# Kernel optimization log

Hardware: AMD Instinct MI355X
Metric: run time of the kernel (lower is better)

Reference implementation:

```python
import jax, jax.numpy as jnp
import numpy as np

NUM_ITERATIONS = 5
USE_SYMMETRIC_FINAL = True


def setup_inputs() -> dict:
    key = jax.random.key(0)
    k1, _ = jax.random.split(key)
    log_scores = jax.random.normal(k1, (4, 16, 1024, 1024), dtype=jnp.float32)
    tau = jnp.float32(1.0)
    return {"log_scores": log_scores, "tau": tau}


def reference(log_scores, tau):
    # tau clamped to min 0.1 as in torch .clamp(min=0.1)
    tau_c = jnp.maximum(tau, jnp.float32(0.1))
    ls = log_scores / tau_c
    # Sinkhorn iterations: alternate row / column logsumexp normalization.
    for _ in range(NUM_ITERATIONS):
        ls = ls - jax.nn.logsumexp(ls, axis=-1, keepdims=True)  # row normalize
        ls = ls - jax.nn.logsumexp(ls, axis=-2, keepdims=True)  # col normalize
    if USE_SYMMETRIC_FINAL:
        ls = ls - jax.nn.logsumexp(ls, axis=-1, keepdims=True)
        ls_col = ls - jax.nn.logsumexp(ls, axis=-2, keepdims=True)
        ls = 0.5 * (ls + ls_col)
    return jnp.exp(ls)
```

## Files before the change

kernel.cpp:

```cpp
#include <hip/hip_runtime.h>
#include <hip/hip_fp16.h>


#define NROWS 1024
#define NCOLS 1024
#define NMAT 64
#define MATELEMS (NROWS * NCOLS)

struct H8 { __half2 h[4]; };

__device__ __forceinline__ float wave_sum(float v) {
#pragma unroll
  for (int o = 32; o > 0; o >>= 1) v += __shfl_xor(v, o, 64);
  return v;
}

__global__ __launch_bounds__(256) void convert_row(
    const float* __restrict__ x, __half* __restrict__ t,
    float* __restrict__ r, const float* __restrict__ tau) {
  const float it = 1.0f / fmaxf(tau[0], 0.1f);
  const int row = blockIdx.x * 4 + (threadIdx.x >> 6);
  const int lane = threadIdx.x & 63;
  const float4* xr = (const float4*)(x + (size_t)row * NCOLS);
  H8* tr = (H8*)(t + (size_t)row * NCOLS);
  float s = 0.0f;
#pragma unroll
  for (int k = 0; k < 2; ++k) {
    const int f4 = k * 128 + lane * 2;
    float4 a = xr[f4];
    float4 b = xr[f4 + 1];
    a.x *= it; a.y *= it; a.z *= it; a.w *= it;
    b.x *= it; b.y *= it; b.z *= it; b.w *= it;
    H8 o;
    o.h[0] = __floats2half2_rn(a.x, a.y);
    o.h[1] = __floats2half2_rn(a.z, a.w);
    o.h[2] = __floats2half2_rn(b.x, b.y);
    o.h[3] = __floats2half2_rn(b.z, b.w);
    tr[k * 64 + lane] = o;
    s += __expf(a.x) + __expf(a.y) + __expf(a.z) + __expf(a.w) +
         __expf(b.x) + __expf(b.y) + __expf(b.z) + __expf(b.w);
  }
  s = wave_sum(s);
  if (lane == 0) r[row] = __logf(s);
}

__global__ __launch_bounds__(256) void row_pass(
    const __half* __restrict__ t, const float* __restrict__ c,
    float* __restrict__ r) {
  const int row = blockIdx.x * 4 + (threadIdx.x >> 6);
  const int lane = threadIdx.x & 63;
  const int mat = row >> 10;
  const H8* tr = (const H8*)(t + (size_t)row * NCOLS);
  const float4* cm = (const float4*)(c + mat * NCOLS);
  float s = 0.0f;
#pragma unroll
  for (int k = 0; k < 2; ++k) {
    H8 v = tr[k * 64 + lane];
    const int f4 = k * 128 + lane * 2;
    float4 c0 = cm[f4];
    float4 c1 = cm[f4 + 1];
    float2 f0 = __half22float2(v.h[0]);
    float2 f1 = __half22float2(v.h[1]);
    float2 f2 = __half22float2(v.h[2]);
    float2 f3 = __half22float2(v.h[3]);
    s += __expf(f0.x - c0.x) + __expf(f0.y - c0.y) +
         __expf(f1.x - c0.z) + __expf(f1.y - c0.w) +
         __expf(f2.x - c1.x) + __expf(f2.y - c1.y) +
         __expf(f3.x - c1.z) + __expf(f3.y - c1.w);
  }
  s = wave_sum(s);
  if (lane == 0) r[row] = __logf(s);
}

template <int FUSE>
__global__ __launch_bounds__(256) void col_pass(
    const __half* __restrict__ t, const float* __restrict__ r,
    const float* __restrict__ cin, float* __restrict__ cout,
    float* __restrict__ out) {
  const int mat = blockIdx.x >> 3;
  const int cb = blockIdx.x & 7;
  const int colh = threadIdx.x & 15;
  const int rg = threadIdx.x >> 4;
  const int h8idx = cb * 16 + colh;
  const __half* tb = t + (size_t)mat * MATELEMS;
  const float* rb = r + mat * NROWS;

  float s[8];
#pragma unroll
  for (int j = 0; j < 8; ++j) s[j] = 0.0f;

  for (int rr = 0; rr < 64; ++rr) {
    const int row = rg * 64 + rr;
    H8 v = ((const H8*)(tb + (size_t)row * NCOLS))[h8idx];
    const float ri = rb[row];
#pragma unroll
    for (int j = 0; j < 4; ++j) {
      float2 f = __half22float2(v.h[j]);
      s[2 * j] += __expf(f.x - ri);
      s[2 * j + 1] += __expf(f.y - ri);
    }
  }

  __shared__ float ls[16][128];
  __shared__ float hs[128];
#pragma unroll
  for (int j = 0; j < 8; ++j) ls[rg][colh * 8 + j] = s[j];
  __syncthreads();

  if (threadIdx.x < 128) {
    float acc = 0.0f;
#pragma unroll
    for (int g = 0; g < 16; ++g) acc += ls[g][threadIdx.x];
    const float lse = __logf(acc);
    if (FUSE) {
      hs[threadIdx.x] = 0.5f * (lse + cin[mat * NCOLS + cb * 128 + threadIdx.x]);
    } else {
      cout[mat * NCOLS + cb * 128 + threadIdx.x] = lse;
    }
  }

  if (FUSE) {
    __syncthreads();
    float h[8];
#pragma unroll
    for (int j = 0; j < 8; ++j) h[j] = hs[colh * 8 + j];
    float* ob = out + (size_t)mat * MATELEMS;
    for (int rr = 0; rr < 64; ++rr) {
      const int row = rg * 64 + rr;
      H8 v = ((const H8*)(tb + (size_t)row * NCOLS))[h8idx];
      const float ri = rb[row];
      float4 o0, o1;
      float2 f0 = __half22float2(v.h[0]);
      float2 f1 = __half22float2(v.h[1]);
      float2 f2 = __half22float2(v.h[2]);
      float2 f3 = __half22float2(v.h[3]);
      o0.x = __expf(f0.x - ri - h[0]);
      o0.y = __expf(f0.y - ri - h[1]);
      o0.z = __expf(f1.x - ri - h[2]);
      o0.w = __expf(f1.y - ri - h[3]);
      o1.x = __expf(f2.x - ri - h[4]);
      o1.y = __expf(f2.y - ri - h[5]);
      o1.z = __expf(f3.x - ri - h[6]);
      o1.w = __expf(f3.y - ri - h[7]);
      float4* op = (float4*)(ob + (size_t)row * NCOLS) + h8idx * 2;
      op[0] = o0;
      op[1] = o1;
    }
  }
}

extern "C" void kernel_launch(void* const* d_in, const int* in_sizes, int n_in,
                              void* d_out, int out_size, void* d_ws,
                              size_t ws_size, hipStream_t stream) {
  const float* x = (const float*)d_in[0];
  const float* tau = (const float*)d_in[1];
  float* out = (float*)d_out;

  __half* t = (__half*)d_ws;
  float* r = (float*)((char*)d_ws + (size_t)NMAT * MATELEMS * sizeof(__half));
  float* c = r + NMAT * NROWS;

  const int row_grid = NMAT * NROWS / 4;
  const int col_grid = NMAT * 8;

  convert_row<<<row_grid, 256, 0, stream>>>(x, t, r, tau);
  for (int i = 0; i < 5; ++i) {
    col_pass<0><<<col_grid, 256, 0, stream>>>(t, r, nullptr, c, nullptr);
    row_pass<<<row_grid, 256, 0, stream>>>(t, c, r);
  }
  col_pass<1><<<col_grid, 256, 0, stream>>>(t, r, c, nullptr, out);
}
```

Baseline: 734.1 us.

## Fuse row pass into column pass via LDS stripe tile and partial row sums

```diff
diff --git a/kernel.cpp b/kernel.cpp
--- a/kernel.cpp
+++ b/kernel.cpp
@@ -6,8 +6,11 @@
 #define NCOLS 1024
 #define NMAT 64
 #define MATELEMS (NROWS * NCOLS)
+#define NSTRIPE 16
+#define SCOLS 64
+#define SH8 8
 
-struct H8 { __half2 h[4]; };
+struct __align__(16) H8 { __half2 h[4]; };
 
 __device__ __forceinline__ float wave_sum(float v) {
 #pragma unroll
@@ -17,7 +20,7 @@
 
 __global__ __launch_bounds__(256) void convert_row(
     const float* __restrict__ x, __half* __restrict__ t,
-    float* __restrict__ r, const float* __restrict__ tau) {
+    float* __restrict__ S, const float* __restrict__ tau) {
   const float it = 1.0f / fmaxf(tau[0], 0.1f);
   const int row = blockIdx.x * 4 + (threadIdx.x >> 6);
   const int lane = threadIdx.x & 63;
@@ -41,99 +44,113 @@
          __expf(b.x) + __expf(b.y) + __expf(b.z) + __expf(b.w);
   }
   s = wave_sum(s);
-  if (lane == 0) r[row] = __logf(s);
+  if (lane == 0) S[row] = s;
 }
 
-__global__ __launch_bounds__(256) void row_pass(
-    const __half* __restrict__ t, const float* __restrict__ c,
-    float* __restrict__ r) {
-  const int row = blockIdx.x * 4 + (threadIdx.x >> 6);
-  const int lane = threadIdx.x & 63;
-  const int mat = row >> 10;
-  const H8* tr = (const H8*)(t + (size_t)row * NCOLS);
-  const float4* cm = (const float4*)(c + mat * NCOLS);
-  float s = 0.0f;
+template <int FINAL>
+__global__ __launch_bounds__(1024) void fused_col(
+    const __half* __restrict__ t, const float* __restrict__ Pin, const int ns,
+    const float* __restrict__ cin, float* __restrict__ cout,
+    float* __restrict__ Pout, float* __restrict__ out) {
+  const int mat = blockIdx.x >> 4;
+  const int sb = blockIdx.x & 15;
+  const int tid = threadIdx.x;
+  const __half* tb = t + (size_t)mat * MATELEMS + sb * SCOLS;
+
+  __shared__ H8 tile[NROWS * SH8];
+  __shared__ float r_lds[NROWS];
+  __shared__ float wred[16][SCOLS];
+  __shared__ float c_lds[SCOLS];
+
+  {
+    const float* pb = Pin + (size_t)mat * ns * NROWS + tid;
+    float acc = 0.0f;
+    for (int s2 = 0; s2 < ns; ++s2) acc += pb[s2 * NROWS];
+    r_lds[tid] = __logf(acc);
+  }
+  __syncthreads();
+
+  const int c8 = tid & 7;
+  const int rowg = tid >> 3;
+  float s[8];
 #pragma unroll
-  for (int k = 0; k < 2; ++k) {
-    H8 v = tr[k * 64 + lane];
-    const int f4 = k * 128 + lane * 2;
-    float4 c0 = cm[f4];
-    float4 c1 = cm[f4 + 1];
+  for (int j = 0; j < 8; ++j) s[j] = 0.0f;
+#pragma unroll
+  for (int ch = 0; ch < 8; ++ch) {
+    const int row = ch * 128 + rowg;
+    H8 v = ((const H8*)(tb + (size_t)row * NCOLS))[c8];
+    tile[row * SH8 + (c8 ^ (row & 7))] = v;
+    const float ri = r_lds[row];
     float2 f0 = __half22float2(v.h[0]);
     float2 f1 = __half22float2(v.h[1]);
     float2 f2 = __half22float2(v.h[2]);
     float2 f3 = __half22float2(v.h[3]);
-    s += __expf(f0.x - c0.x) + __expf(f0.y - c0.y) +
-         __expf(f1.x - c0.z) + __expf(f1.y - c0.w) +
-         __expf(f2.x - c1.x) + __expf(f2.y - c1.y) +
-         __expf(f3.x - c1.z) + __expf(f3.y - c1.w);
+    s[0] += __expf(f0.x - ri); s[1] += __expf(f0.y - ri);
+    s[2] += __expf(f1.x - ri); s[3] += __expf(f1.y - ri);
+    s[4] += __expf(f2.x - ri); s[5] += __expf(f2.y - ri);
+    s[6] += __expf(f3.x - ri); s[7] += __expf(f3.y - ri);
   }
-  s = wave_sum(s);
-  if (lane == 0) r[row] = __logf(s);
-}
-
-template <int FUSE>
-__global__ __launch_bounds__(256) void col_pass(
-    const __half* __restrict__ t, const float* __restrict__ r,
-    const float* __restrict__ cin, float* __restrict__ cout,
-    float* __restrict__ out) {
-  const int mat = blockIdx.x >> 3;
-  const int cb = blockIdx.x & 7;
-  const int colh = threadIdx.x & 15;
-  const int rg = threadIdx.x >> 4;
-  const int h8idx = cb * 16 + colh;
-  const __half* tb = t + (size_t)mat * MATELEMS;
-  const float* rb = r + mat * NROWS;
-
-  float s[8];
 #pragma unroll
-  for (int j = 0; j < 8; ++j) s[j] = 0.0f;
-
-  for (int rr = 0; rr < 64; ++rr) {
-    const int row = rg * 64 + rr;
-    H8 v = ((const H8*)(tb + (size_t)row * NCOLS))[h8idx];
-    const float ri = rb[row];
+  for (int j = 0; j < 8; ++j) {
+    s[j] += __shfl_xor(s[j], 8, 64);
+    s[j] += __shfl_xor(s[j], 16, 64);
+    s[j] += __shfl_xor(s[j], 32, 64);
+  }
+  if ((tid & 63) < 8) {
+    const int wv = tid >> 6;
 #pragma unroll
-    for (int j = 0; j < 4; ++j) {
-      float2 f = __half22float2(v.h[j]);
-      s[2 * j] += __expf(f.x - ri);
-      s[2 * j + 1] += __expf(f.y - ri);
+    for (int j = 0; j < 8; ++j) wred[wv][c8 * 8 + j] = s[j];
+  }
+  __syncthreads();
+  if (tid < SCOLS) {
+    float acc = 0.0f;
+#pragma unroll
+    for (int w = 0; w < 16; ++w) acc += wred[w][tid];
+    const float lse = __logf(acc);
+    if (FINAL) {
+      c_lds[tid] = 0.5f * (lse + cin[mat * NCOLS + sb * SCOLS + tid]);
+    } else {
+      c_lds[tid] = lse;
+      cout[mat * NCOLS + sb * SCOLS + tid] = lse;
     }
   }
-
-  __shared__ float ls[16][128];
-  __shared__ float hs[128];
-#pragma unroll
-  for (int j = 0; j < 8; ++j) ls[rg][colh * 8 + j] = s[j];
   __syncthreads();
 
-  if (threadIdx.x < 128) {
-    float acc = 0.0f;
+  if (!FINAL) {
+    const int row = tid;
+    const int sw = row & 7;
+    float rp0 = 0.0f, rp1 = 0.0f;
 #pragma unroll
-    for (int g = 0; g < 16; ++g) acc += ls[g][threadIdx.x];
-    const float lse = __logf(acc);
-    if (FUSE) {
-      hs[threadIdx.x] = 0.5f * (lse + cin[mat * NCOLS + cb * 128 + threadIdx.x]);
-    } else {
-      cout[mat * NCOLS + cb * 128 + threadIdx.x] = lse;
-    }
-  }
-
-  if (FUSE) {
-    __syncthreads();
-    float h[8];
-#pragma unroll
-    for (int j = 0; j < 8; ++j) h[j] = hs[colh * 8 + j];
-    float* ob = out + (size_t)mat * MATELEMS;
-    for (int rr = 0; rr < 64; ++rr) {
-      const int row = rg * 64 + rr;
-      H8 v = ((const H8*)(tb + (size_t)row * NCOLS))[h8idx];
-      const float ri = rb[row];
-      float4 o0, o1;
+    for (int g = 0; g < 8; ++g) {
+      H8 v = tile[row * SH8 + (g ^ sw)];
       float2 f0 = __half22float2(v.h[0]);
       float2 f1 = __half22float2(v.h[1]);
       float2 f2 = __half22float2(v.h[2]);
       float2 f3 = __half22float2(v.h[3]);
+      const float* cj = &c_lds[g * 8];
+      rp0 += __expf(f0.x - cj[0]) + __expf(f0.y - cj[1]) +
+             __expf(f1.x - cj[2]) + __expf(f1.y - cj[3]);
+      rp1 += __expf(f2.x - cj[4]) + __expf(f2.y - cj[5]) +
+             __expf(f3.x - cj[6]) + __expf(f3.y - cj[7]);
+    }
+    Pout[((size_t)mat * NSTRIPE + sb) * NROWS + row] = rp0 + rp1;
+  } else {
+    const int colh = tid & 7;
+    const int rg = tid >> 3;
+    float h[8];
+#pragma unroll
+    for (int j = 0; j < 8; ++j) h[j] = c_lds[colh * 8 + j];
+    float* ob = out + (size_t)mat * MATELEMS + sb * SCOLS;
+#pragma unroll
+    for (int ch = 0; ch < 8; ++ch) {
+      const int row = ch * 128 + rg;
+      H8 v = tile[row * SH8 + (colh ^ (row & 7))];
+      const float ri = r_lds[row];
+      float2 f0 = __half22float2(v.h[0]);
+      float2 f1 = __half22float2(v.h[1]);
+      float2 f2 = __half22float2(v.h[2]);
+      float2 f3 = __half22float2(v.h[3]);
+      float4 o0, o1;
       o0.x = __expf(f0.x - ri - h[0]);
       o0.y = __expf(f0.y - ri - h[1]);
       o0.z = __expf(f1.x - ri - h[2]);
@@ -142,7 +159,7 @@
       o1.y = __expf(f2.y - ri - h[5]);
       o1.z = __expf(f3.x - ri - h[6]);
       o1.w = __expf(f3.y - ri - h[7]);
-      float4* op = (float4*)(ob + (size_t)row * NCOLS) + h8idx * 2;
+      float4* op = (float4*)(ob + (size_t)row * NCOLS) + colh * 2;
       op[0] = o0;
       op[1] = o1;
     }
@@ -157,16 +174,19 @@
   float* out = (float*)d_out;
 
   __half* t = (__half*)d_ws;
-  float* r = (float*)((char*)d_ws + (size_t)NMAT * MATELEMS * sizeof(__half));
-  float* c = r + NMAT * NROWS;
+  float* S1 = (float*)((char*)d_ws + (size_t)NMAT * MATELEMS * sizeof(__half));
+  float* PA = S1 + NMAT * NROWS;
+  float* PB = PA + NMAT * NSTRIPE * NROWS;
+  float* c = PB + NMAT * NSTRIPE * NROWS;
 
   const int row_grid = NMAT * NROWS / 4;
-  const int col_grid = NMAT * 8;
+  const int f_grid = NMAT * NSTRIPE;
 
-  convert_row<<<row_grid, 256, 0, stream>>>(x, t, r, tau);
-  for (int i = 0; i < 5; ++i) {
-    col_pass<0><<<col_grid, 256, 0, stream>>>(t, r, nullptr, c, nullptr);
-    row_pass<<<row_grid, 256, 0, stream>>>(t, c, r);
-  }
-  col_pass<1><<<col_grid, 256, 0, stream>>>(t, r, c, nullptr, out);
+  convert_row<<<row_grid, 256, 0, stream>>>(x, t, S1, tau);
+  fused_col<0><<<f_grid, 1024, 0, stream>>>(t, S1, 1, nullptr, c, PA, nullptr);
+  fused_col<0><<<f_grid, 1024, 0, stream>>>(t, PA, NSTRIPE, nullptr, c, PB, nullptr);
+  fused_col<0><<<f_grid, 1024, 0, stream>>>(t, PB, NSTRIPE, nullptr, c, PA, nullptr);
+  fused_col<0><<<f_grid, 1024, 0, stream>>>(t, PA, NSTRIPE, nullptr, c, PB, nullptr);
+  fused_col<0><<<f_grid, 1024, 0, stream>>>(t, PB, NSTRIPE, nullptr, c, PA, nullptr);
+  fused_col<1><<<f_grid, 1024, 0, stream>>>(t, PA, NSTRIPE, c, nullptr, nullptr, out);
 }
```

Result: no change. 745.8 us (+1.6%).
